# Performance work log

Measured on AMD Instinct MI355X. Metric: run time of the kernel, lower is better.

The kernel has to match this reference:

```python
import jax, jax.numpy as jnp
import numpy as np


def setup_inputs() -> dict:
    key = jax.random.key(0)
    ks = jax.random.split(key, 9)
    N, C, H, W, K = 8, 512, 64, 64, 32
    C4 = C // 4
    s = lambda k, shape, scale=0.02: jax.random.normal(k, shape, dtype=jnp.float32) * scale
    return {
        "x": jax.random.normal(ks[0], (N, C, H, W), dtype=jnp.float32),
        "y": jax.random.normal(ks[1], (N, K, C), dtype=jnp.float32),
        "wq": s(ks[2], (C4, C)),
        "bq": s(ks[3], (C4,)),
        "wk": s(ks[4], (C4, C)),
        "bk": s(ks[5], (C4,)),
        "wv": s(ks[6], (C, C)),
        "bv": s(ks[7], (C,)),
        "scale": s(ks[8], (1,), 1.0),
    }


def reference(x, y, wq, bq, wk, bk, wv, bv, scale):
    N, C, H, W = x.shape
    # 1x1 conv query: (N,C,H,W) -> (N,C4,H,W) -> (N, HW, C4)
    q = jnp.einsum('nchw,oc->nhwo', x, wq) + bq  # (N,H,W,C4)
    q = q.reshape(N, H * W, -1)                   # (N, HW, C4)
    # key/value linears on centers y: (N,K,C)
    k = y @ wk.T + bk                             # (N, K, C4)
    v = y @ wv.T + bv                             # (N, K, C)
    energy = jnp.einsum('npc,nkc->npk', q, k)     # (N, HW, K)
    attn = jax.nn.softmax(energy, axis=-1)
    out = jnp.einsum('nkc,npk->ncp', v, attn)     # (N, C, HW)
    out = out.reshape(N, C, H, W)
    return scale[0] * out + x
```

## Files before the change

kernel.cpp:

```cpp
#include <hip/hip_runtime.h>


#define N_  8
#define C_  512
#define HW_ 4096
#define K_  32

typedef __attribute__((ext_vector_type(8))) short bf16x8;
typedef __attribute__((ext_vector_type(4))) float f32x4;
typedef __attribute__((ext_vector_type(2))) int i32x2;
typedef __attribute__((ext_vector_type(4))) int i32x4;

__device__ __forceinline__ unsigned short f2b(float f) {
    union { float f; unsigned u; } v; v.f = f;
    unsigned r = v.u + 0x7FFFu + ((v.u >> 16) & 1u);
    return (unsigned short)(r >> 16);
}
__device__ __forceinline__ float b2f(unsigned short h) {
    union { unsigned u; float f; } v; v.u = ((unsigned)h) << 16; return v.f;
}

__device__ __forceinline__ int wqk_idx(int kk, int c) {
    return ((((c >> 5) * 2 + (kk >> 4)) * 64 + ((c >> 3) & 3) * 16 + (kk & 15)) << 3) + (c & 7);
}

__global__ __launch_bounds__(256) void prep_kernel(
    const float* __restrict__ y, const float* __restrict__ wq, const float* __restrict__ bq,
    const float* __restrict__ wk, const float* __restrict__ bk,
    const float* __restrict__ wv, const float* __restrict__ bv,
    unsigned short* __restrict__ wqkf, float* __restrict__ bqk, unsigned short* __restrict__ vtf)
{
    const int bid = blockIdx.x;
    const int t = threadIdx.x;

    if (bid < 256) {
        __shared__ float vred[3][4][16][8];
        const int n   = bid >> 5;
        const int ct  = bid & 31;
        const int cl  = t & 15;
        const int kko = (t >> 4) & 3;
        const int jq4 = t >> 6;
        const int c   = ct * 16 + cl;

        const float* yb  = y  + ((size_t)n * K_ + kko * 8) * C_ + jq4 * 128;
        const float* wvb = wv + (size_t)c * C_ + jq4 * 128;
        float acc[8] = {0,0,0,0,0,0,0,0};
        #pragma unroll 4
        for (int jj = 0; jj < 32; ++jj) {
            float4 w4 = *(const float4*)(wvb + jj * 4);
            #pragma unroll
            for (int u = 0; u < 8; ++u) {
                float4 y4 = *(const float4*)(yb + (size_t)u * C_ + jj * 4);
                acc[u] += y4.x * w4.x + y4.y * w4.y + y4.z * w4.z + y4.w * w4.w;
            }
        }
        if (jq4 > 0) {
            #pragma unroll
            for (int u = 0; u < 8; ++u) vred[jq4 - 1][kko][cl][u] = acc[u];
        }
        __syncthreads();
        if (jq4 == 0) {
            const float bvc = bv[c];
            unsigned short o[8];
            #pragma unroll
            for (int u = 0; u < 8; ++u) {
                float s = acc[u] + vred[0][kko][cl][u] + vred[1][kko][cl][u]
                        + vred[2][kko][cl][u] + bvc;
                o[u] = f2b(s);
            }
            i32x4 pk = { (int)(o[0] | ((unsigned)o[1] << 16)), (int)(o[2] | ((unsigned)o[3] << 16)),
                         (int)(o[4] | ((unsigned)o[5] << 16)), (int)(o[6] | ((unsigned)o[7] << 16)) };
            *(i32x4*)(vtf + (size_t)n * (K_ * C_) + (size_t)((ct * 64 + kko * 16 + cl) * 8)) = pk;
        }
    } else {
        __shared__ __align__(16) float kp[2][128];
        __shared__ __align__(16) float kr[128];
        const int b = bid - 256;
        const int n = b >> 5, kk = b & 31;
        const int o = t & 127, half = t >> 7;

        const float* yb  = y  + ((size_t)n * K_ + kk) * C_ + half * 256;
        const float* wkb = wk + (size_t)o * C_ + half * 256;
        float a = 0.f;
        #pragma unroll 4
        for (int jq = 0; jq < 64; ++jq) {
            float4 w4 = *(const float4*)(wkb + jq * 4);
            float4 y4 = *(const float4*)(yb + jq * 4);
            a += y4.x * w4.x + y4.y * w4.y + y4.z * w4.z + y4.w * w4.w;
        }
        kp[half][o] = a;
        __syncthreads();
        if (t < 128) kr[t] = kp[0][t] + kp[1][t] + bk[t];
        __syncthreads();
        if (t < 64) {
            float s = kr[t] * bq[t] + kr[t + 64] * bq[t + 64];
            #pragma unroll
            for (int d = 32; d > 0; d >>= 1) s += __shfl_down(s, d);
            if (t == 0) bqk[n * K_ + kk] = s;
        }
        const int c1 = t, c2 = t + 256;
        float s1 = 0.f, s2 = 0.f;
        for (int oq = 0; oq < 32; ++oq) {
            float4 k4 = *(const float4*)(&kr[oq * 4]);
            const float* wq0 = wq + (size_t)(oq * 4) * C_;
            s1 += k4.x * wq0[c1] + k4.y * wq0[C_ + c1] + k4.z * wq0[2*C_ + c1] + k4.w * wq0[3*C_ + c1];
            s2 += k4.x * wq0[c2] + k4.y * wq0[C_ + c2] + k4.z * wq0[2*C_ + c2] + k4.w * wq0[3*C_ + c2];
        }
        unsigned short* wqf_n = wqkf + (size_t)n * (K_ * C_);
        wqf_n[wqk_idx(kk, c1)] = f2b(s1);
        wqf_n[wqk_idx(kk, c2)] = f2b(s2);
    }
}

__global__ __launch_bounds__(256) void main_kernel(
    const float* __restrict__ x, const unsigned short* __restrict__ wqkf,
    const unsigned short* __restrict__ vtf, const float* __restrict__ bqk,
    const float* __restrict__ scale, float* __restrict__ out)
{
    __shared__ __align__(16) unsigned short xl[17408];
    __shared__ float e_lds[32][33];

    const int bid = (blockIdx.x & 7) * 128 + (blockIdx.x >> 3);
    const int n  = bid >> 7;
    const int p0 = (bid & 127) * 32;
    const int t  = threadIdx.x;
    const int w  = t >> 6, l = t & 63;
    const int l15 = l & 15, lg = l >> 4;
    const float* xg = x + (size_t)n * C_ * HW_;
    float* og = out + (size_t)n * C_ * HW_;
    const unsigned short* wqf  = wqkf + (size_t)n * (K_ * C_);
    const unsigned short* vtfn = vtf  + (size_t)n * (K_ * C_);

    const int mh = w;
    const int kt = w >> 1;
    bf16x8 vf[8];
    #pragma unroll
    for (int mi = 0; mi < 8; ++mi)
        vf[mi] = *(const bf16x8*)(vtfn + ((size_t)(mh * 8 + mi) * 64 + l) * 8);
    bf16x8 b0 = *(const bf16x8*)(wqf + ((size_t)(0 * 2 + kt) * 64 + l) * 8);
    bf16x8 b1 = *(const bf16x8*)(wqf + ((size_t)(1 * 2 + kt) * 64 + l) * 8);

    {
        const float* xp0 = xg + p0;
        const int px4 = (t & 7) * 4;
        const int crow = t >> 3;
        const int pxh = ((px4 >> 4) & 1) * 64 + (px4 & 15);
        const int crowpart = ((crow >> 3) & 3) * 272 + ((crow >> 2) & 1) * 128
                           + (crow & 3) * 16 + pxh;

        float4 ra[4], rb[4];
        #pragma unroll
        for (int u = 0; u < 4; ++u)
            ra[u] = *(const float4*)(xp0 + (size_t)(u * 32 + crow) * HW_ + px4);
        for (int b = 0; b < 4; ++b) {
            if (b < 3) {
                #pragma unroll
                for (int u = 0; u < 4; ++u)
                    rb[u] = *(const float4*)(xp0 + (size_t)((b + 1) * 128 + u * 32 + crow) * HW_ + px4);
            }
            #pragma unroll
            for (int u = 0; u < 4; ++u) {
                const float4 r = ra[u];
                const int elem = (b * 4 + u) * 1088 + crowpart;
                i32x2 pk = { (int)(f2b(r.x) | ((unsigned)f2b(r.y) << 16)),
                             (int)(f2b(r.z) | ((unsigned)f2b(r.w) << 16)) };
                *(i32x2*)(xl + elem) = pk;
            }
            #pragma unroll
            for (int u = 0; u < 4; ++u) ra[u] = rb[u];
        }
    }
    __syncthreads();

    {
        const int pt = w & 1;
        f32x4 acc = {0.f, 0.f, 0.f, 0.f};
        for (int cs = 0; cs < 16; ++cs) {
            bf16x8 b2;
            if (cs < 14) b2 = *(const bf16x8*)(wqf + ((size_t)((cs + 2) * 2 + kt) * 64 + l) * 8);
            const unsigned short* xp = xl + cs * 1088 + lg * 272 + pt * 64 + l15;
            const unsigned e0 = xp[0],   e1 = xp[16],  e2 = xp[32],  e3 = xp[48];
            const unsigned e4 = xp[128], e5 = xp[144], e6 = xp[160], e7 = xp[176];
            union { unsigned u[4]; bf16x8 v; } af;
            af.u[0] = e0 | (e1 << 16);  af.u[1] = e2 | (e3 << 16);
            af.u[2] = e4 | (e5 << 16);  af.u[3] = e6 | (e7 << 16);
            acc = __builtin_amdgcn_mfma_f32_16x16x32_bf16(af.v, b0, acc, 0, 0, 0);
            b0 = b1; b1 = b2;
        }
        const float bq_ = bqk[n * K_ + kt * 16 + l15];
        #pragma unroll
        for (int r = 0; r < 4; ++r)
            e_lds[pt * 16 + lg * 4 + r][kt * 16 + l15] = acc[r] + bq_;
    }
    __syncthreads();

    bf16x8 paf0, paf1;
    {
        const float* er0 = e_lds[l15];
        const float* er1 = e_lds[16 + l15];
        float e0[32], e1[32];
        #pragma unroll
        for (int k = 0; k < 32; ++k) { e0[k] = er0[k]; e1[k] = er1[k]; }
        float m0 = e0[0], m1 = e1[0];
        #pragma unroll
        for (int k = 1; k < 32; ++k) { m0 = fmaxf(m0, e0[k]); m1 = fmaxf(m1, e1[k]); }
        float s0 = 0.f, s1 = 0.f;
        #pragma unroll
        for (int k = 0; k < 32; ++k) {
            e0[k] = __expf(e0[k] - m0); s0 += e0[k];
            e1[k] = __expf(e1[k] - m1); s1 += e1[k];
        }
        const float i0 = 1.f / s0, i1 = 1.f / s1;
        #pragma unroll
        for (int j = 0; j < 8; ++j) {
            paf0[j] = (short)f2b(e0[8 * lg + j] * i0);
            paf1[j] = (short)f2b(e1[8 * lg + j] * i1);
        }
    }

    {
        const float fs = scale[0];
        const int pxa = p0 + l15, pxb = p0 + 16 + l15;
        const int mt0 = mh * 8;

        #pragma unroll
        for (int mi = 0; mi < 8; ++mi) {
            const int mt = mt0 + mi;
            f32x4 d0 = __builtin_amdgcn_mfma_f32_16x16x32_bf16(vf[mi], paf0, (f32x4){0.f,0.f,0.f,0.f}, 0, 0, 0);
            f32x4 d1 = __builtin_amdgcn_mfma_f32_16x16x32_bf16(vf[mi], paf1, (f32x4){0.f,0.f,0.f,0.f}, 0, 0, 0);
            const int base = (mt >> 1) * 1088 + ((mt & 1) * 2 + (lg >> 1)) * 272
                           + (lg & 1) * 128 + l15;
            const int cc = mt * 16 + lg * 4;
            #pragma unroll
            for (int r = 0; r < 4; ++r) {
                const float xa0 = b2f(xl[base + r * 16]);
                const float xa1 = b2f(xl[base + r * 16 + 64]);
                og[(size_t)(cc + r) * HW_ + pxa] = fs * d0[r] + xa0;
                og[(size_t)(cc + r) * HW_ + pxb] = fs * d1[r] + xa1;
            }
        }
    }
}

extern "C" void kernel_launch(void* const* d_in, const int* in_sizes, int n_in,
                              void* d_out, int out_size, void* d_ws, size_t ws_size,
                              hipStream_t stream) {
    const float* x     = (const float*)d_in[0];
    const float* y     = (const float*)d_in[1];
    const float* wq    = (const float*)d_in[2];
    const float* bq    = (const float*)d_in[3];
    const float* wk    = (const float*)d_in[4];
    const float* bk    = (const float*)d_in[5];
    const float* wv    = (const float*)d_in[6];
    const float* bv    = (const float*)d_in[7];
    const float* scale = (const float*)d_in[8];

    unsigned short* wqkf = (unsigned short*)d_ws;
    unsigned short* vtf  = wqkf + (size_t)N_ * K_ * C_;
    float* bqk = (float*)((char*)d_ws + 524288);

    prep_kernel<<<512, 256, 0, stream>>>(y, wq, bq, wk, bk, wv, bv, wqkf, bqk, vtf);
    main_kernel<<<1024, 256, 0, stream>>>(x, wqkf, vtf, bqk, scale, (float*)d_out);
}
```

Before: 58.82 us.

## Re-layout x tile in LDS to pixel-major with channel-packed 16-byte vectors

Changes the shared-memory layout of the bf16 x tile so that each pixel holds 8 consecutive channels contiguously. The MFMA A-operand can then be fetched with a single 128-bit LDS read instead of eight scalar reads plus packing, and the residual reads become 64-bit vector loads. The global load pattern changes to scalar per-pixel loads over 8 channels (32 consecutive pixels per channel row) instead of float4 loads, and padding is removed, which could increase bank conflicts on the 16-byte writes.

```diff
diff --git a/kernel.cpp b/kernel.cpp
--- a/kernel.cpp
+++ b/kernel.cpp
@@ -8,6 +8,7 @@
 
 typedef __attribute__((ext_vector_type(8))) short bf16x8;
 typedef __attribute__((ext_vector_type(4))) float f32x4;
+typedef __attribute__((ext_vector_type(4))) unsigned short u16x4;
 typedef __attribute__((ext_vector_type(2))) int i32x2;
 typedef __attribute__((ext_vector_type(4))) int i32x4;
 
@@ -117,7 +118,7 @@
     const unsigned short* __restrict__ vtf, const float* __restrict__ bqk,
     const float* __restrict__ scale, float* __restrict__ out)
 {
-    __shared__ __align__(16) unsigned short xl[17408];
+    __shared__ __align__(16) unsigned short xl[16384];
     __shared__ float e_lds[32][33];
 
     const int bid = (blockIdx.x & 7) * 128 + (blockIdx.x >> 3);
@@ -141,50 +142,40 @@
     bf16x8 b1 = *(const bf16x8*)(wqf + ((size_t)(1 * 2 + kt) * 64 + l) * 8);
 
     {
-        const float* xp0 = xg + p0;
-        const int px4 = (t & 7) * 4;
-        const int crow = t >> 3;
-        const int pxh = ((px4 >> 4) & 1) * 64 + (px4 & 15);
-        const int crowpart = ((crow >> 3) & 3) * 272 + ((crow >> 2) & 1) * 128
-                           + (crow & 3) * 16 + pxh;
-
-        float4 ra[4], rb[4];
-        #pragma unroll
-        for (int u = 0; u < 4; ++u)
-            ra[u] = *(const float4*)(xp0 + (size_t)(u * 32 + crow) * HW_ + px4);
-        for (int b = 0; b < 4; ++b) {
-            if (b < 3) {
+        const int px = t & 31, g = t >> 5;
+        const float* xc = xg + p0 + px;
+        float ra[8], rb[8];
+        #pragma unroll
+        for (int j = 0; j < 8; ++j) ra[j] = xc[(size_t)(g * 8 + j) * HW_];
+        for (int u = 0; u < 8; ++u) {
+            if (u < 7) {
                 #pragma unroll
-                for (int u = 0; u < 4; ++u)
-                    rb[u] = *(const float4*)(xp0 + (size_t)((b + 1) * 128 + u * 32 + crow) * HW_ + px4);
-            }
-            #pragma unroll
-            for (int u = 0; u < 4; ++u) {
-                const float4 r = ra[u];
-                const int elem = (b * 4 + u) * 1088 + crowpart;
-                i32x2 pk = { (int)(f2b(r.x) | ((unsigned)f2b(r.y) << 16)),
-                             (int)(f2b(r.z) | ((unsigned)f2b(r.w) << 16)) };
-                *(i32x2*)(xl + elem) = pk;
-            }
-            #pragma unroll
-            for (int u = 0; u < 4; ++u) ra[u] = rb[u];
+                for (int j = 0; j < 8; ++j)
+                    rb[j] = xc[(size_t)(g * 8 + (u + 1) * 64 + j) * HW_];
+            }
+            unsigned short o[8];
+            #pragma unroll
+            for (int j = 0; j < 8; ++j) o[j] = f2b(ra[j]);
+            const int cbase = g * 8 + u * 64;
+            const int elem = ((cbase >> 5) * 1024) + (((cbase >> 3) & 3) * 256) + px * 8;
+            i32x4 pk = { (int)(o[0] | ((unsigned)o[1] << 16)), (int)(o[2] | ((unsigned)o[3] << 16)),
+                         (int)(o[4] | ((unsigned)o[5] << 16)), (int)(o[6] | ((unsigned)o[7] << 16)) };
+            *(i32x4*)(xl + elem) = pk;
+            #pragma unroll
+            for (int j = 0; j < 8; ++j) ra[j] = rb[j];
         }
     }
     __syncthreads();
 
     {
         const int pt = w & 1;
+        const unsigned short* xbase = xl + lg * 256 + (pt * 16 + l15) * 8;
         f32x4 acc = {0.f, 0.f, 0.f, 0.f};
         for (int cs = 0; cs < 16; ++cs) {
             bf16x8 b2;
             if (cs < 14) b2 = *(const bf16x8*)(wqf + ((size_t)((cs + 2) * 2 + kt) * 64 + l) * 8);
-            const unsigned short* xp = xl + cs * 1088 + lg * 272 + pt * 64 + l15;
-            const unsigned e0 = xp[0],   e1 = xp[16],  e2 = xp[32],  e3 = xp[48];
-            const unsigned e4 = xp[128], e5 = xp[144], e6 = xp[160], e7 = xp[176];
-            union { unsigned u[4]; bf16x8 v; } af;
-            af.u[0] = e0 | (e1 << 16);  af.u[1] = e2 | (e3 << 16);
-            af.u[2] = e4 | (e5 << 16);  af.u[3] = e6 | (e7 << 16);
-            acc = __builtin_amdgcn_mfma_f32_16x16x32_bf16(af.v, b0, acc, 0, 0, 0);
+            const bf16x8 af = *(const bf16x8*)(xbase + cs * 1024);
+            acc = __builtin_amdgcn_mfma_f32_16x16x32_bf16(af, b0, acc, 0, 0, 0);
             b0 = b1; b1 = b2;
         }
         const float bq_ = bqk[n * K_ + kt * 16 + l15];
@@ -228,15 +219,14 @@
             const int mt = mt0 + mi;
             f32x4 d0 = __builtin_amdgcn_mfma_f32_16x16x32_bf16(vf[mi], paf0, (f32x4){0.f,0.f,0.f,0.f}, 0, 0, 0);
             f32x4 d1 = __builtin_amdgcn_mfma_f32_16x16x32_bf16(vf[mi], paf1, (f32x4){0.f,0.f,0.f,0.f}, 0, 0, 0);
-            const int base = (mt >> 1) * 1088 + ((mt & 1) * 2 + (lg >> 1)) * 272
-                           + (lg & 1) * 128 + l15;
+            const int base = (mt >> 1) * 1024 + ((2 * mt + (lg >> 1)) & 3) * 256 + (lg & 1) * 4;
+            const u16x4 ra = *(const u16x4*)(xl + base + l15 * 8);
+            const u16x4 rb = *(const u16x4*)(xl + base + (16 + l15) * 8);
             const int cc = mt * 16 + lg * 4;
             #pragma unroll
             for (int r = 0; r < 4; ++r) {
-                const float xa0 = b2f(xl[base + r * 16]);
-                const float xa1 = b2f(xl[base + r * 16 + 64]);
-                og[(size_t)(cc + r) * HW_ + pxa] = fs * d0[r] + xa0;
-                og[(size_t)(cc + r) * HW_ + pxb] = fs * d1[r] + xa1;
+                og[(size_t)(cc + r) * HW_ + pxa] = fs * d0[r] + b2f(ra[r]);
+                og[(size_t)(cc + r) * HW_ + pxb] = fs * d1[r] + b2f(rb[r]);
             }
         }
     }
```

After: 58.60 us. No clear change (-0.4%).
